# Kernel tuning notes

Measured on AMD Instinct MI355X. Metric: run time of the kernel, lower is better.

Reference implementation:

```python
import jax, jax.numpy as jnp
import numpy as np

N = 100000   # nodes
E = 1280000  # edges
D = 64       # emb_dim
L = 5        # num_layers
G = 512      # graphs in batch
AF, AV = 9, 120  # atom feature columns / vocab
BF, BV = 3, 6    # bond feature columns / vocab
BN_EPS = 1e-5


def setup_inputs() -> dict:
    key = jax.random.key(0)
    ks = jax.random.split(key, 12)
    inp = {
        'x_feats': jax.random.randint(ks[0], (N, AF), 0, AV),
        'edge_index': jax.random.randint(ks[1], (2, E), 0, N),
        'edge_attr': jax.random.randint(ks[2], (E, BF), 0, BV),
        'batch': jnp.sort(jax.random.randint(ks[3], (N,), 0, G)),
        # AtomEncoder: one embedding table per atom feature column
        'atom_emb': 0.02 * jax.random.normal(ks[4], (AF, AV, D), jnp.float32),
        # per-layer BondEncoder tables
        'bond_emb': 0.02 * jax.random.normal(ks[5], (L, BF, BV, D), jnp.float32),
        'eps': jnp.zeros((L,), jnp.float32),                 # GIN eps per layer
        'W1': 0.05 * jax.random.normal(ks[6], (L, D, D), jnp.float32),
        'b1': jnp.zeros((L, D), jnp.float32),
        'bn1_g': jnp.ones((L, D), jnp.float32),
        'bn1_b': jnp.zeros((L, D), jnp.float32),
        'W2': 0.05 * jax.random.normal(ks[7], (L, D, D), jnp.float32),
        'b2': jnp.zeros((L, D), jnp.float32),
        'bn_g': jnp.ones((L, D), jnp.float32),
        'bn_b': jnp.zeros((L, D), jnp.float32),
    }
    return inp


def _batchnorm(h, g, b):
    # training-mode batch statistics over the node dimension (biased var, as torch)
    m = h.mean(axis=0)
    v = jnp.mean((h - m) ** 2, axis=0)
    return (h - m) * jax.lax.rsqrt(v + BN_EPS) * g + b


def reference(atom_emb, bond_emb, eps, W1, b1, bn1_g, bn1_b, W2, b2, bn_g, bn_b,
              x_feats, edge_index, edge_attr, batch):
    # AtomEncoder: sum of per-column embeddings -> [N, D]
    h = sum(atom_emb[f][x_feats[:, f]] for f in range(AF))
    row, col = edge_index[0], edge_index[1]  # source, target (PyG source_to_target)
    fp_list = []
    for l in range(L):
        # BondEncoder for this layer -> [E, D]
        e = sum(bond_emb[l, f][edge_attr[:, f]] for f in range(BF))
        # GIN message: relu(x_j + edge_emb), scatter-add to targets
        msg = jax.nn.relu(h[row] + e)
        agg = jax.ops.segment_sum(msg, col, num_segments=N)
        z = (1.0 + eps[l]) * h + agg
        # MLP: Linear -> BN -> ReLU -> Linear
        z = z @ W1[l] + b1[l]
        z = jax.nn.relu(_batchnorm(z, bn1_g[l], bn1_b[l]))
        z = z @ W2[l] + b2[l]
        # outer batchnorm; dropout is identity in eval mode
        h = _batchnorm(z, bn_g[l], bn_b[l])
        if l != L - 1:
            h = jax.nn.relu(h)
        fp_list.append(jax.ops.segment_sum(h, batch, num_segments=G))
    node_representation = h  # JK='last'
    fp_emb = jnp.stack(fp_list, axis=1)  # [G, L, D]
    return node_representation, fp_emb
```

## Files before the change

### kernel.cpp

```cpp
#include <hip/hip_runtime.h>

#define DD 64
#define LL 5
#define GG 512
#define AFN 9
#define AVN 120
#define BFN 3
#define BVN 6
#define BNEPS 1e-5f
#define SCB 1024

typedef unsigned int uint;
typedef unsigned short ushort;
typedef short bhalf8 __attribute__((ext_vector_type(8)));
typedef float fx4 __attribute__((ext_vector_type(4)));

__device__ inline ushort f2bf(float f) {
  uint u = __float_as_uint(f);
  uint r = (u + 0x7FFF + ((u >> 16) & 1)) >> 16;
  return (ushort)r;
}
__device__ inline float bf2f(ushort u) { return __uint_as_float(((uint)u) << 16); }

__global__ __launch_bounds__(256) void k_atom(
    const int* __restrict__ xf, const float* __restrict__ aemb,
    ushort* __restrict__ h2, int N)
{
  int t = blockIdx.x * 256 + threadIdx.x;
  int row = t >> 4, c4 = t & 15;
  if (row >= N) return;
  const int* x = xf + row * AFN;
  float4 s = make_float4(0.f, 0.f, 0.f, 0.f);
  #pragma unroll
  for (int f = 0; f < AFN; ++f) {
    int v = x[f];
    float4 w = ((const float4*)aemb)[(f * AVN + v) * 16 + c4];
    s.x += w.x; s.y += w.y; s.z += w.z; s.w += w.w;
  }
  ushort4 p;
  p.x = f2bf(s.x); p.y = f2bf(s.y); p.z = f2bf(s.z); p.w = f2bf(s.w);
  ((ushort4*)h2)[row * 16 + c4] = p;
}

__global__ __launch_bounds__(256) void k_hist(const int* __restrict__ ei,
    int* __restrict__ deg, int* __restrict__ rank, int E)
{
  int t = blockIdx.x * 256 + threadIdx.x;
  if (t >= E) return;
  rank[t] = atomicAdd(&deg[ei[E + t]], 1);
}

__global__ __launch_bounds__(1024) void k_scan1(const int* __restrict__ deg,
    int* __restrict__ scanned, int* __restrict__ bsum, int N)
{
  __shared__ int s[SCB];
  int i = blockIdx.x * SCB + threadIdx.x;
  int x = (i < N) ? deg[i] : 0;
  s[threadIdx.x] = x;
  for (int off = 1; off < SCB; off <<= 1) {
    __syncthreads();
    int v = (threadIdx.x >= off) ? s[threadIdx.x - off] : 0;
    __syncthreads();
    s[threadIdx.x] += v;
  }
  __syncthreads();
  if (i < N) scanned[i] = s[threadIdx.x] - x;
  if (threadIdx.x == SCB - 1) bsum[blockIdx.x] = s[SCB - 1];
}

__global__ __launch_bounds__(128) void k_scan2(const int* __restrict__ bsum,
    int* __restrict__ boff, int NB)
{
  __shared__ int s[128];
  int x = (threadIdx.x < NB) ? bsum[threadIdx.x] : 0;
  s[threadIdx.x] = x;
  for (int off = 1; off < 128; off <<= 1) {
    __syncthreads();
    int v = (threadIdx.x >= off) ? s[threadIdx.x - off] : 0;
    __syncthreads();
    s[threadIdx.x] += v;
  }
  __syncthreads();
  if (threadIdx.x < NB) boff[threadIdx.x] = s[threadIdx.x] - x;
}

__global__ __launch_bounds__(256) void k_fill(const int* __restrict__ ei,
    const int* __restrict__ ea, const int* __restrict__ scanned,
    const int* __restrict__ boff, const int* __restrict__ rank,
    int* __restrict__ rcarr, int E)
{
  int t = blockIdx.x * 256 + threadIdx.x;
  if (t >= E) return;
  int r = ei[t], c = ei[E + t];
  int code = ea[t * 3 + 0] + ea[t * 3 + 1] * 6 + ea[t * 3 + 2] * 36;
  int pos = scanned[c] + boff[c >> 10] + rank[t];
  rcarr[pos] = r | (code << 20);
}

__global__ __launch_bounds__(256) void k_bcomb(const float* __restrict__ bemb,
    float* __restrict__ bcomb)
{
  int t = blockIdx.x * 256 + threadIdx.x;
  if (t >= LL * 216 * DD) return;
  int ch = t & 63;
  int cl = t >> 6;
  int code = cl % 216;
  int l = cl / 216;
  int a0 = code % 6, a1 = (code / 6) % 6, a2 = code / 36;
  const float* B = bemb + (size_t)l * BFN * BVN * DD;
  bcomb[t] = B[(0 * BVN + a0) * DD + ch] + B[(1 * BVN + a1) * DD + ch]
           + B[(2 * BVN + a2) * DD + ch];
}

__global__ __launch_bounds__(256) void k_bounds(const int* __restrict__ batch,
    int* __restrict__ gs, int N)
{
  int g = blockIdx.x * 256 + threadIdx.x;
  if (g > GG) return;
  int lo = 0, hi = N;
  while (lo < hi) { int mid = (lo + hi) >> 1; if (batch[mid] < g) lo = mid + 1; else hi = mid; }
  gs[g] = lo;
}

__global__ __launch_bounds__(256) void k_wprep(const float* __restrict__ W1,
    const float* __restrict__ W2, ushort* __restrict__ wfrag)
{
  int t = blockIdx.x * 256 + threadIdx.x;
  if (t >= LL * 2 * 4096) return;
  int r = t & 7;
  int lane = (t >> 3) & 63;
  int kb = (t >> 9) & 1;
  int jt = (t >> 10) & 3;
  int wsel = (t >> 12) & 1;
  int l = t >> 13;
  int k = kb * 32 + ((lane >> 4) & 3) * 8 + r;
  int j = jt * 16 + (lane & 15);
  const float* Ws = (wsel ? W2 : W1) + (size_t)l * DD * DD;
  wfrag[t] = f2bf(Ws[k * DD + j]);
}

__global__ __launch_bounds__(256) void k_gather(
    const ushort* __restrict__ h2, const int* __restrict__ rcarr,
    const int* __restrict__ scanned, const int* __restrict__ boff,
    const float* __restrict__ bc, float* __restrict__ agg, int N, int E)
{
  int lane = threadIdx.x & 63;
  int node = blockIdx.x * 4 + (threadIdx.x >> 6);
  if (node >= N) return;
  int s = scanned[node] + boff[node >> 10];
  int e = (node + 1 < N) ? (scanned[node + 1] + boff[(node + 1) >> 10]) : E;
  int sub = lane >> 4;
  int c4 = lane & 15;
  float a0 = 0.f, a1 = 0.f, a2 = 0.f, a3 = 0.f;
  const uint2* h2v = (const uint2*)h2;
  const float4* bc4 = (const float4*)bc;
  for (int k0 = s; k0 < e; k0 += 4) {
    int idx = k0 + sub;
    bool valid = idx < e;
    int rck = rcarr[valid ? idx : s];
    int r = rck & 0xFFFFF;
    int code = (rck >> 20) & 0xFFF;
    uint2 hv = h2v[r * 16 + c4];
    float4 bv = bc4[code * 16 + c4];
    float f0 = __uint_as_float(hv.x << 16);
    float f1 = __uint_as_float(hv.x & 0xFFFF0000u);
    float f2 = __uint_as_float(hv.y << 16);
    float f3 = __uint_as_float(hv.y & 0xFFFF0000u);
    float m0 = fmaxf(f0 + bv.x, 0.f);
    float m1 = fmaxf(f1 + bv.y, 0.f);
    float m2 = fmaxf(f2 + bv.z, 0.f);
    float m3 = fmaxf(f3 + bv.w, 0.f);
    if (valid) { a0 += m0; a1 += m1; a2 += m2; a3 += m3; }
  }
  a0 += __shfl_xor(a0, 16); a1 += __shfl_xor(a1, 16);
  a2 += __shfl_xor(a2, 16); a3 += __shfl_xor(a3, 16);
  a0 += __shfl_xor(a0, 32); a1 += __shfl_xor(a1, 32);
  a2 += __shfl_xor(a2, 32); a3 += __shfl_xor(a3, 32);
  if (sub == 0)
    ((float4*)agg)[(size_t)node * 16 + c4] = make_float4(a0, a1, a2, a3);
}

__global__ __launch_bounds__(256) void k_mlpA(
    const ushort* __restrict__ h2, const float* __restrict__ agg,
    const ushort* __restrict__ wfrag, const float* __restrict__ bvec,
    const float* __restrict__ epsl, ushort* __restrict__ z1b,
    float* __restrict__ stats, int NT, int nwaves)
{
  __shared__ float sred[128];
  __shared__ ushort ldsT[4][16][72];
  if (threadIdx.x < 128) sred[threadIdx.x] = 0.f;
  __syncthreads();
  int lane = threadIdx.x & 63;
  int wid = threadIdx.x >> 6;
  int gwave = blockIdx.x * 4 + wid;
  int hi = lane >> 4, lo = lane & 15;
  float epsv = 1.f + epsl[0];
  bhalf8 af[8];
  #pragma unroll
  for (int f = 0; f < 8; ++f)
    af[f] = *(const bhalf8*)(wfrag + f * 512 + lane * 8);
  float4 bq[4];
  #pragma unroll
  for (int jt = 0; jt < 4; ++jt)
    bq[jt] = *(const float4*)(bvec + jt * 16 + hi * 4);
  float sS[4][4] = {{0}}, sQ[4][4] = {{0}};
  for (int mt = gwave; mt < NT; mt += nwaves) {
    int node = mt * 16 + lo;
    const ushort* hrow = h2 + (size_t)node * DD;
    const float* arow = agg + (size_t)node * DD;
    bhalf8 bfr[2];
    #pragma unroll
    for (int kb = 0; kb < 2; ++kb) {
      int k0 = kb * 32 + hi * 8;
      uint4 hv = *(const uint4*)(hrow + k0);
      float4 aa = *(const float4*)(arow + k0);
      float4 ab = *(const float4*)(arow + k0 + 4);
      float xr[8];
      xr[0] = fmaf(epsv, __uint_as_float(hv.x << 16), aa.x);
      xr[1] = fmaf(epsv, __uint_as_float(hv.x & 0xFFFF0000u), aa.y);
      xr[2] = fmaf(epsv, __uint_as_float(hv.y << 16), aa.z);
      xr[3] = fmaf(epsv, __uint_as_float(hv.y & 0xFFFF0000u), aa.w);
      xr[4] = fmaf(epsv, __uint_as_float(hv.z << 16), ab.x);
      xr[5] = fmaf(epsv, __uint_as_float(hv.z & 0xFFFF0000u), ab.y);
      xr[6] = fmaf(epsv, __uint_as_float(hv.w << 16), ab.z);
      xr[7] = fmaf(epsv, __uint_as_float(hv.w & 0xFFFF0000u), ab.w);
      bhalf8 b8;
      #pragma unroll
      for (int r = 0; r < 8; ++r) b8[r] = (short)f2bf(xr[r]);
      bfr[kb] = b8;
    }
    fx4 acc[4];
    #pragma unroll
    for (int jt = 0; jt < 4; ++jt) {
      fx4 a = {0.f, 0.f, 0.f, 0.f};
      a = __builtin_amdgcn_mfma_f32_16x16x32_bf16(af[jt * 2 + 0], bfr[0], a, 0, 0, 0);
      a = __builtin_amdgcn_mfma_f32_16x16x32_bf16(af[jt * 2 + 1], bfr[1], a, 0, 0, 0);
      acc[jt] = a;
    }
    #pragma unroll
    for (int jt = 0; jt < 4; ++jt) {
      float z0 = acc[jt][0] + bq[jt].x;
      float z1 = acc[jt][1] + bq[jt].y;
      float z2 = acc[jt][2] + bq[jt].z;
      float z3 = acc[jt][3] + bq[jt].w;
      sS[jt][0] += z0; sQ[jt][0] += z0 * z0;
      sS[jt][1] += z1; sQ[jt][1] += z1 * z1;
      sS[jt][2] += z2; sQ[jt][2] += z2 * z2;
      sS[jt][3] += z3; sQ[jt][3] += z3 * z3;
      uint p0 = ((uint)f2bf(z1) << 16) | f2bf(z0);
      uint p1 = ((uint)f2bf(z3) << 16) | f2bf(z2);
      int jphys = jt ^ (lo & 3);
      *(uint2*)&ldsT[wid][lo][jphys * 16 + hi * 4] = make_uint2(p0, p1);
    }
    int row = lane >> 2, pch = lane & 3;
    int pphys = pch ^ (row & 3);
    const uint4* src = (const uint4*)&ldsT[wid][row][pphys * 16];
    uint4 v0 = src[0], v1 = src[1];
    uint4* dst = (uint4*)(z1b + ((size_t)(mt * 16 + row)) * DD + pch * 16);
    dst[0] = v0; dst[1] = v1;
  }
  #pragma unroll
  for (int o = 1; o < 16; o <<= 1)
    #pragma unroll
    for (int jt = 0; jt < 4; ++jt)
      #pragma unroll
      for (int q = 0; q < 4; ++q) {
        sS[jt][q] += __shfl_xor(sS[jt][q], o);
        sQ[jt][q] += __shfl_xor(sQ[jt][q], o);
      }
  if (lo == 0) {
    #pragma unroll
    for (int jt = 0; jt < 4; ++jt)
      #pragma unroll
      for (int q = 0; q < 4; ++q) {
        atomicAdd(&sred[jt * 16 + hi * 4 + q], sS[jt][q]);
        atomicAdd(&sred[64 + jt * 16 + hi * 4 + q], sQ[jt][q]);
      }
  }
  __syncthreads();
  if (threadIdx.x < 128) atomicAdd(&stats[threadIdx.x], sred[threadIdx.x]);
}

__global__ __launch_bounds__(256) void k_mlpB(
    ushort* __restrict__ z1b, const ushort* __restrict__ wfrag,
    const float* __restrict__ bvec, const float* __restrict__ g1,
    const float* __restrict__ b1g, const float* __restrict__ statsIn,
    float* __restrict__ statsOut, float invN, int NT, int nwaves)
{
  __shared__ float sred[128];
  __shared__ float scl[DD], shl[DD];
  __shared__ ushort ldsT[4][16][72];
  if (threadIdx.x < 128) sred[threadIdx.x] = 0.f;
  if (threadIdx.x < DD) {
    int j = threadIdx.x;
    float m = statsIn[j] * invN;
    float v = statsIn[DD + j] * invN - m * m;
    float sc = rsqrtf(v + BNEPS) * g1[j];
    scl[j] = sc;
    shl[j] = b1g[j] - m * sc;
  }
  __syncthreads();
  int lane = threadIdx.x & 63;
  int wid = threadIdx.x >> 6;
  int gwave = blockIdx.x * 4 + wid;
  int hi = lane >> 4, lo = lane & 15;
  bhalf8 af[8];
  #pragma unroll
  for (int f = 0; f < 8; ++f)
    af[f] = *(const bhalf8*)(wfrag + f * 512 + lane * 8);
  float4 bq[4];
  #pragma unroll
  for (int jt = 0; jt < 4; ++jt)
    bq[jt] = *(const float4*)(bvec + jt * 16 + hi * 4);
  float4 scr[2][2], shr[2][2];
  #pragma unroll
  for (int kb = 0; kb < 2; ++kb) {
    int k0 = kb * 32 + hi * 8;
    scr[kb][0] = *(const float4*)&scl[k0];
    scr[kb][1] = *(const float4*)&scl[k0 + 4];
    shr[kb][0] = *(const float4*)&shl[k0];
    shr[kb][1] = *(const float4*)&shl[k0 + 4];
  }
  float sS[4][4] = {{0}}, sQ[4][4] = {{0}};
  for (int mt = gwave; mt < NT; mt += nwaves) {
    int node = mt * 16 + lo;
    const ushort* zrow = z1b + (size_t)node * DD;
    bhalf8 bfr[2];
    #pragma unroll
    for (int kb = 0; kb < 2; ++kb) {
      int k0 = kb * 32 + hi * 8;
      uint4 zv = *(const uint4*)(zrow + k0);
      float xr[8];
      xr[0] = __uint_as_float(zv.x << 16);
      xr[1] = __uint_as_float(zv.x & 0xFFFF0000u);
      xr[2] = __uint_as_float(zv.y << 16);
      xr[3] = __uint_as_float(zv.y & 0xFFFF0000u);
      xr[4] = __uint_as_float(zv.z << 16);
      xr[5] = __uint_as_float(zv.z & 0xFFFF0000u);
      xr[6] = __uint_as_float(zv.w << 16);
      xr[7] = __uint_as_float(zv.w & 0xFFFF0000u);
      xr[0] = fmaxf(fmaf(xr[0], scr[kb][0].x, shr[kb][0].x), 0.f);
      xr[1] = fmaxf(fmaf(xr[1], scr[kb][0].y, shr[kb][0].y), 0.f);
      xr[2] = fmaxf(fmaf(xr[2], scr[kb][0].z, shr[kb][0].z), 0.f);
      xr[3] = fmaxf(fmaf(xr[3], scr[kb][0].w, shr[kb][0].w), 0.f);
      xr[4] = fmaxf(fmaf(xr[4], scr[kb][1].x, shr[kb][1].x), 0.f);
      xr[5] = fmaxf(fmaf(xr[5], scr[kb][1].y, shr[kb][1].y), 0.f);
      xr[6] = fmaxf(fmaf(xr[6], scr[kb][1].z, shr[kb][1].z), 0.f);
      xr[7] = fmaxf(fmaf(xr[7], scr[kb][1].w, shr[kb][1].w), 0.f);
      bhalf8 b8;
      #pragma unroll
      for (int r = 0; r < 8; ++r) b8[r] = (short)f2bf(xr[r]);
      bfr[kb] = b8;
    }
    fx4 acc[4];
    #pragma unroll
    for (int jt = 0; jt < 4; ++jt) {
      fx4 a = {0.f, 0.f, 0.f, 0.f};
      a = __builtin_amdgcn_mfma_f32_16x16x32_bf16(af[jt * 2 + 0], bfr[0], a, 0, 0, 0);
      a = __builtin_amdgcn_mfma_f32_16x16x32_bf16(af[jt * 2 + 1], bfr[1], a, 0, 0, 0);
      acc[jt] = a;
    }
    #pragma unroll
    for (int jt = 0; jt < 4; ++jt) {
      float z0 = acc[jt][0] + bq[jt].x;
      float z1 = acc[jt][1] + bq[jt].y;
      float z2 = acc[jt][2] + bq[jt].z;
      float z3 = acc[jt][3] + bq[jt].w;
      sS[jt][0] += z0; sQ[jt][0] += z0 * z0;
      sS[jt][1] += z1; sQ[jt][1] += z1 * z1;
      sS[jt][2] += z2; sQ[jt][2] += z2 * z2;
      sS[jt][3] += z3; sQ[jt][3] += z3 * z3;
      uint p0 = ((uint)f2bf(z1) << 16) | f2bf(z0);
      uint p1 = ((uint)f2bf(z3) << 16) | f2bf(z2);
      int jphys = jt ^ (lo & 3);
      *(uint2*)&ldsT[wid][lo][jphys * 16 + hi * 4] = make_uint2(p0, p1);
    }
    int row = lane >> 2, pch = lane & 3;
    int pphys = pch ^ (row & 3);
    const uint4* src = (const uint4*)&ldsT[wid][row][pphys * 16];
    uint4 v0 = src[0], v1 = src[1];
    uint4* dst = (uint4*)(z1b + ((size_t)(mt * 16 + row)) * DD + pch * 16);
    dst[0] = v0; dst[1] = v1;
  }
  #pragma unroll
  for (int o = 1; o < 16; o <<= 1)
    #pragma unroll
    for (int jt = 0; jt < 4; ++jt)
      #pragma unroll
      for (int q = 0; q < 4; ++q) {
        sS[jt][q] += __shfl_xor(sS[jt][q], o);
        sQ[jt][q] += __shfl_xor(sQ[jt][q], o);
      }
  if (lo == 0) {
    #pragma unroll
    for (int jt = 0; jt < 4; ++jt)
      #pragma unroll
      for (int q = 0; q < 4; ++q) {
        atomicAdd(&sred[jt * 16 + hi * 4 + q], sS[jt][q]);
        atomicAdd(&sred[64 + jt * 16 + hi * 4 + q], sQ[jt][q]);
      }
  }
  __syncthreads();
  if (threadIdx.x < 128) atomicAdd(&statsOut[threadIdx.x], sred[threadIdx.x]);
}

__global__ __launch_bounds__(256) void k_bnout_fp(
    const ushort* __restrict__ zb, ushort* __restrict__ h2,
    const float* __restrict__ g2, const float* __restrict__ b2g,
    const float* __restrict__ statsIn, const int* __restrict__ gs,
    float* __restrict__ fp, float* __restrict__ outp,
    int l, float invN)
{
  __shared__ float sc[DD], sh[DD], part[4 * DD];
  int tid = threadIdx.x;
  if (tid < DD) {
    float m = statsIn[tid] * invN;
    float v = statsIn[DD + tid] * invN - m * m;
    float inv = rsqrtf(v + BNEPS);
    float scale = inv * g2[tid];
    sc[tid] = scale;
    sh[tid] = b2g[tid] - m * scale;
  }
  __syncthreads();
  int g = blockIdx.x;
  int r0 = gs[g], r1 = gs[g + 1];
  int ch = tid & 63, rg = tid >> 6;
  bool last = (l == LL - 1);
  float facc = 0.f;
  for (int r = r0 + rg; r < r1; r += 4) {
    float z = bf2f(zb[(size_t)r * DD + ch]);
    float y = z * sc[ch] + sh[ch];
    if (!last) y = fmaxf(y, 0.f);
    h2[(size_t)r * DD + ch] = f2bf(y);
    if (last) outp[(size_t)r * DD + ch] = y;
    facc += y;
  }
  part[rg * DD + ch] = facc;
  __syncthreads();
  if (tid < DD) {
    float s = part[tid] + part[DD + tid] + part[2 * DD + tid] + part[3 * DD + tid];
    fp[((size_t)g * LL + l) * DD + tid] = s;
  }
}

extern "C" void kernel_launch(void* const* d_in, const int* in_sizes, int n_in,
                              void* d_out, int out_size, void* d_ws, size_t ws_size,
                              hipStream_t stream)
{
  const int*   x_feats    = (const int*)d_in[0];
  const int*   edge_index = (const int*)d_in[1];
  const int*   edge_attr  = (const int*)d_in[2];
  const int*   batch      = (const int*)d_in[3];
  const float* atom_emb   = (const float*)d_in[4];
  const float* bond_emb   = (const float*)d_in[5];
  const float* eps        = (const float*)d_in[6];
  const float* W1         = (const float*)d_in[7];
  const float* b1         = (const float*)d_in[8];
  const float* bn1_g      = (const float*)d_in[9];
  const float* bn1_b      = (const float*)d_in[10];
  const float* W2         = (const float*)d_in[11];
  const float* b2         = (const float*)d_in[12];
  const float* bn_g       = (const float*)d_in[13];
  const float* bn_b       = (const float*)d_in[14];

  int N = in_sizes[3];
  int E = in_sizes[1] / 2;
  int NB = (N + SCB - 1) / SCB;
  int NT = N >> 4;
  float invN = 1.f / (float)N;

  float* out = (float*)d_out;
  float* fp  = out + (size_t)N * DD;

  float* buf     = (float*)d_ws;
  float* stats   = buf + (size_t)N * DD;
  float* bcomb   = stats + LL * 256;
  ushort* h2     = (ushort*)(bcomb + LL * 216 * DD);
  ushort* z1b    = h2 + (size_t)N * DD;
  ushort* wfrag  = z1b + (size_t)N * DD;
  int* deg       = (int*)(wfrag + LL * 2 * 4096);
  int* rank      = deg + N;
  int* scanned   = rank + E;
  int* bsum      = scanned + N;
  int* boff      = bsum + 128;
  int* gs        = boff + 128;
  int* rcarr     = gs + (GG + 1);

  hipMemsetAsync(stats, 0, LL * 256 * sizeof(float), stream);
  hipMemsetAsync(deg, 0, (size_t)N * sizeof(int), stream);

  k_atom<<<(N * 16 + 255) / 256, 256, 0, stream>>>(x_feats, atom_emb, h2, N);
  k_hist<<<(E + 255) / 256, 256, 0, stream>>>(edge_index, deg, rank, E);
  k_scan1<<<NB, SCB, 0, stream>>>(deg, scanned, bsum, N);
  k_scan2<<<1, 128, 0, stream>>>(bsum, boff, NB);
  k_fill<<<(E + 255) / 256, 256, 0, stream>>>(edge_index, edge_attr, scanned,
                                              boff, rank, rcarr, E);
  k_bcomb<<<(LL * 216 * DD + 255) / 256, 256, 0, stream>>>(bond_emb, bcomb);
  k_bounds<<<(GG + 256) / 256, 256, 0, stream>>>(batch, gs, N);
  k_wprep<<<(LL * 2 * 4096 + 255) / 256, 256, 0, stream>>>(W1, W2, wfrag);

  const int gridM = 640;
  const int nwaves = gridM * 4;
  for (int l = 0; l < LL; ++l) {
    float* s1 = stats + l * 256;
    float* s2 = s1 + 128;
    k_gather<<<(N + 3) / 4, 256, 0, stream>>>(h2, rcarr, scanned, boff,
                                              bcomb + (size_t)l * 216 * DD, buf, N, E);
    k_mlpA<<<gridM, 256, 0, stream>>>(h2, buf, wfrag + (size_t)(l * 2 + 0) * 4096,
                                      b1 + l * DD, eps + l, z1b, s1, NT, nwaves);
    k_mlpB<<<gridM, 256, 0, stream>>>(z1b, wfrag + (size_t)(l * 2 + 1) * 4096,
                                      b2 + l * DD, bn1_g + l * DD, bn1_b + l * DD,
                                      s1, s2, invN, NT, nwaves);
    k_bnout_fp<<<GG, 256, 0, stream>>>(z1b, h2, bn_g + l * DD, bn_b + l * DD,
                                       s2, gs, fp, out, l, invN);
  }
}
```

Before: 835.6 us.

## Split node features into channel slabs and gather one slab per pass

Node embeddings h2 are stored as four channel slabs of 16 bf16 values each instead of row-major 64-wide rows, and the edge gather runs four passes, one per slab. Each slab is about 3.2 MB, small enough that random neighbour reads can stay resident in L2/MALL cache within a pass. The cost is four launches per layer, re-reading the CSR edge array four times, and narrower 32-byte row fetches. The MLP and BN-output kernels are updated to read and write the slab layout.

```diff
diff --git a/kernel.cpp b/kernel.cpp
--- a/kernel.cpp
+++ b/kernel.cpp
@@ -9,6 +9,8 @@
 #define BVN 6
 #define BNEPS 1e-5f
 #define SCB 1024
+#define NSLAB 4
+#define SCH 16
 
 typedef unsigned int uint;
 typedef unsigned short ushort;
@@ -21,6 +23,7 @@
   return (ushort)r;
 }
 __device__ inline float bf2f(ushort u) { return __uint_as_float(((uint)u) << 16); }
+
 
 __global__ __launch_bounds__(256) void k_atom(
     const int* __restrict__ xf, const float* __restrict__ aemb,
@@ -39,7 +42,9 @@
   }
   ushort4 p;
   p.x = f2bf(s.x); p.y = f2bf(s.y); p.z = f2bf(s.z); p.w = f2bf(s.w);
-  ((ushort4*)h2)[row * 16 + c4] = p;
+  int slab = c4 >> 2;
+  ushort* dst = h2 + (size_t)slab * N * SCH + (size_t)row * SCH + (c4 & 3) * 4;
+  *(ushort4*)dst = p;
 }
 
 __global__ __launch_bounds__(256) void k_hist(const int* __restrict__ ei,
@@ -142,26 +147,27 @@
 __global__ __launch_bounds__(256) void k_gather(
     const ushort* __restrict__ h2, const int* __restrict__ rcarr,
     const int* __restrict__ scanned, const int* __restrict__ boff,
-    const float* __restrict__ bc, float* __restrict__ agg, int N, int E)
+    const float* __restrict__ bc, float* __restrict__ agg,
+    int N, int E, int pass)
 {
   int lane = threadIdx.x & 63;
   int node = blockIdx.x * 4 + (threadIdx.x >> 6);
   if (node >= N) return;
   int s = scanned[node] + boff[node >> 10];
   int e = (node + 1 < N) ? (scanned[node + 1] + boff[(node + 1) >> 10]) : E;
-  int sub = lane >> 4;
-  int c4 = lane & 15;
+  int es = lane >> 2;
+  int chq = lane & 3;
+  const ushort* slab = h2 + (size_t)pass * N * SCH;
+  const float* bcs = bc + pass * SCH;
   float a0 = 0.f, a1 = 0.f, a2 = 0.f, a3 = 0.f;
-  const uint2* h2v = (const uint2*)h2;
-  const float4* bc4 = (const float4*)bc;
-  for (int k0 = s; k0 < e; k0 += 4) {
-    int idx = k0 + sub;
+  for (int k0 = s; k0 < e; k0 += 16) {
+    int idx = k0 + es;
     bool valid = idx < e;
     int rck = rcarr[valid ? idx : s];
     int r = rck & 0xFFFFF;
     int code = (rck >> 20) & 0xFFF;
-    uint2 hv = h2v[r * 16 + c4];
-    float4 bv = bc4[code * 16 + c4];
+    uint2 hv = *(const uint2*)(slab + (size_t)r * SCH + chq * 4);
+    float4 bv = *(const float4*)(bcs + code * DD + chq * 4);
     float f0 = __uint_as_float(hv.x << 16);
     float f1 = __uint_as_float(hv.x & 0xFFFF0000u);
     float f2 = __uint_as_float(hv.y << 16);
@@ -172,19 +178,24 @@
     float m3 = fmaxf(f3 + bv.w, 0.f);
     if (valid) { a0 += m0; a1 += m1; a2 += m2; a3 += m3; }
   }
+  a0 += __shfl_xor(a0, 4);  a1 += __shfl_xor(a1, 4);
+  a2 += __shfl_xor(a2, 4);  a3 += __shfl_xor(a3, 4);
+  a0 += __shfl_xor(a0, 8);  a1 += __shfl_xor(a1, 8);
+  a2 += __shfl_xor(a2, 8);  a3 += __shfl_xor(a3, 8);
   a0 += __shfl_xor(a0, 16); a1 += __shfl_xor(a1, 16);
   a2 += __shfl_xor(a2, 16); a3 += __shfl_xor(a3, 16);
   a0 += __shfl_xor(a0, 32); a1 += __shfl_xor(a1, 32);
   a2 += __shfl_xor(a2, 32); a3 += __shfl_xor(a3, 32);
-  if (sub == 0)
-    ((float4*)agg)[(size_t)node * 16 + c4] = make_float4(a0, a1, a2, a3);
+  if (es == 0)
+    *(float4*)(agg + (size_t)node * DD + pass * SCH + chq * 4) =
+        make_float4(a0, a1, a2, a3);
 }
 
 __global__ __launch_bounds__(256) void k_mlpA(
     const ushort* __restrict__ h2, const float* __restrict__ agg,
     const ushort* __restrict__ wfrag, const float* __restrict__ bvec,
     const float* __restrict__ epsl, ushort* __restrict__ z1b,
-    float* __restrict__ stats, int NT, int nwaves)
+    float* __restrict__ stats, int N, int NT, int nwaves)
 {
   __shared__ float sred[128];
   __shared__ ushort ldsT[4][16][72];
@@ -206,13 +217,13 @@
   float sS[4][4] = {{0}}, sQ[4][4] = {{0}};
   for (int mt = gwave; mt < NT; mt += nwaves) {
     int node = mt * 16 + lo;
-    const ushort* hrow = h2 + (size_t)node * DD;
     const float* arow = agg + (size_t)node * DD;
     bhalf8 bfr[2];
     #pragma unroll
     for (int kb = 0; kb < 2; ++kb) {
       int k0 = kb * 32 + hi * 8;
-      uint4 hv = *(const uint4*)(hrow + k0);
+      const ushort* hp = h2 + (size_t)(k0 >> 4) * N * SCH + (size_t)node * SCH + (k0 & 15);
+      uint4 hv = *(const uint4*)hp;
       float4 aa = *(const float4*)(arow + k0);
       float4 ab = *(const float4*)(arow + k0 + 4);
       float xr[8];
@@ -409,7 +420,7 @@
     const float* __restrict__ g2, const float* __restrict__ b2g,
     const float* __restrict__ statsIn, const int* __restrict__ gs,
     float* __restrict__ fp, float* __restrict__ outp,
-    int l, float invN)
+    int l, float invN, int N)
 {
   __shared__ float sc[DD], sh[DD], part[4 * DD];
   int tid = threadIdx.x;
@@ -426,12 +437,14 @@
   int r0 = gs[g], r1 = gs[g + 1];
   int ch = tid & 63, rg = tid >> 6;
   bool last = (l == LL - 1);
+  int slab = ch >> 4;
+  ushort* hdst = h2 + (size_t)slab * N * SCH + (ch & 15);
   float facc = 0.f;
   for (int r = r0 + rg; r < r1; r += 4) {
     float z = bf2f(zb[(size_t)r * DD + ch]);
     float y = z * sc[ch] + sh[ch];
     if (!last) y = fmaxf(y, 0.f);
-    h2[(size_t)r * DD + ch] = f2bf(y);
+    hdst[(size_t)r * SCH] = f2bf(y);
     if (last) outp[(size_t)r * DD + ch] = y;
     facc += y;
   }
@@ -504,14 +517,16 @@
   for (int l = 0; l < LL; ++l) {
     float* s1 = stats + l * 256;
     float* s2 = s1 + 128;
-    k_gather<<<(N + 3) / 4, 256, 0, stream>>>(h2, rcarr, scanned, boff,
-                                              bcomb + (size_t)l * 216 * DD, buf, N, E);
+    for (int p = 0; p < NSLAB; ++p)
+      k_gather<<<(N + 3) / 4, 256, 0, stream>>>(h2, rcarr, scanned, boff,
+                                                bcomb + (size_t)l * 216 * DD,
+                                                buf, N, E, p);
     k_mlpA<<<gridM, 256, 0, stream>>>(h2, buf, wfrag + (size_t)(l * 2 + 0) * 4096,
-                                      b1 + l * DD, eps + l, z1b, s1, NT, nwaves);
+                                      b1 + l * DD, eps + l, z1b, s1, N, NT, nwaves);
     k_mlpB<<<gridM, 256, 0, stream>>>(z1b, wfrag + (size_t)(l * 2 + 1) * 4096,
                                       b2 + l * DD, bn1_g + l * DD, bn1_b + l * DD,
                                       s1, s2, invN, NT, nwaves);
     k_bnout_fp<<<GG, 256, 0, stream>>>(z1b, h2, bn_g + l * DD, bn_b + l * DD,
-                                       s2, gs, fp, out, l, invN);
-  }
-}
+                                       s2, gs, fp, out, l, invN, N);
+  }
+}
```

New measurement: 1.136 ms. 1.36x slower.
